# Optimization experiments

Hardware: AMD Instinct MI355X
Metric: run time of the kernel (lower is better)

## Reference

```python
import jax, jax.numpy as jnp
import numpy as np

SCALE = 20.0
MAX_Q = 256        # SwiGLUDiv max_quotient
MAX_SHIFT = 32     # SwiGLUShift max_shift
MEM_SIZE = 16777216

# c4 VM opcode numbering (39 opcodes; only these are gated in step)
LEA, IMM, JMP, JSR, BZ, BNZ, ENT, ADJ, LEV, LI, LC, SI, SC, PSH = range(14)
OR, XOR, AND, EQ, NE, LT, GT, LE, GE, SHL, SHR, ADD, SUB, MUL, DIV, MOD = range(14, 30)


def silu(x):
    return x * jax.nn.sigmoid(x)


def silu_threshold(x, s=SCALE):
    d = s * x
    return (silu(d + 0.5 * s) - silu(d - 0.5 * s)) / s


def swiglu_mul(a, b):
    return a * silu(b) - a * silu(-b)


def eq_gate(a, b, s=SCALE):
    diff = a - b
    return silu_threshold(diff + 0.5, s) * silu_threshold(-diff + 0.5, s)


def ge_gate(a, b, s=SCALE):
    return silu_threshold(a - b + 0.5, s)


def gt_gate(a, b, s=SCALE):
    return silu_threshold(a - b - 0.5, s)


def swiglu_div(a, b, s=SCALE):
    # division via quotient enumeration, vectorized over q (torch looped)
    q = jnp.arange(MAX_Q, dtype=jnp.float32)
    t1 = a - q * b + 0.5
    th1 = (silu(s * (t1 + 0.5)) - silu(s * (t1 - 0.5))) / s
    t2 = a - (q + 1.0) * b + 0.5
    th2 = (silu(s * (t2 + 0.5)) - silu(s * (t2 - 0.5))) / s
    return jnp.sum((th1 - th2) * q)


def _pulse(x, c):
    d = x - c
    return swiglu_mul(silu_threshold(d + 0.5), silu_threshold(-d + 0.5))


def left_shift(a, b):
    i = jnp.arange(MAX_SHIFT, dtype=jnp.float32)
    powers = 2.0 ** i
    return jnp.sum(swiglu_mul(a, powers) * _pulse(b, i))


def right_shift(a, b):
    i = jnp.arange(MAX_SHIFT, dtype=jnp.float32)
    powers = 2.0 ** i
    return jnp.sum(jnp.floor(a / powers) * _pulse(b, i))


def read_memory(memory, addr):
    # soft-attention read: torch looped over memory positions; vectorized here
    pos = jnp.arange(memory.shape[0], dtype=jnp.float32)
    w = eq_gate(addr, pos)
    w = w / (w.sum() + 1e-8)
    return jnp.sum(w * memory)


def write_memory(memory, addr, value):
    # soft-scatter write: lerp each slot by its address gate
    pos = jnp.arange(memory.shape[0], dtype=jnp.float32)
    g = eq_gate(addr, pos)
    return memory * (1.0 - g) + value * g


def _step(pc, sp, bp, ax, memory):
    pc, sp, bp, ax = (pc.astype(jnp.float32), sp.astype(jnp.float32),
                      bp.astype(jnp.float32), ax.astype(jnp.float32))
    memory = memory.astype(jnp.float32)

    instruction = read_memory(memory, pc)
    opcode = jnp.remainder(instruction, 256.0)
    imm = jnp.floor(instruction / 256.0)
    pc_next = pc + 8.0
    stack_top = read_memory(memory, sp)

    add_result = stack_top + ax
    sub_result = stack_top - ax
    mul_result = swiglu_mul(stack_top, ax)
    ax_safe = ax + eq_gate(ax, 0.0)
    div_result = swiglu_div(stack_top, ax_safe)
    mod_result = stack_top - swiglu_mul(div_result, ax_safe)
    shl_result = left_shift(stack_top, ax)
    shr_result = right_shift(stack_top, ax)
    or_result = stack_top + ax - swiglu_mul(stack_top, ax)
    xor_result = stack_top + ax - 2.0 * swiglu_mul(stack_top, ax)
    and_result = swiglu_mul(stack_top, ax)
    eq_result = eq_gate(stack_top, ax)
    ne_result = 1.0 - eq_gate(stack_top, ax)
    lt_result = gt_gate(ax, stack_top)
    gt_result = gt_gate(stack_top, ax)
    le_result = ge_gate(ax, stack_top)
    ge_result = ge_gate(stack_top, ax)
    li_result = read_memory(memory, ax)
    lc_result = read_memory(memory, ax)
    lea_result = bp + imm

    g = lambda op: eq_gate(opcode, float(op))
    g_lea, g_imm, g_li, g_lc = g(LEA), g(IMM), g(LI), g(LC)
    g_add, g_sub, g_mul, g_div, g_mod = g(ADD), g(SUB), g(MUL), g(DIV), g(MOD)
    g_shl, g_shr, g_or, g_xor, g_and = g(SHL), g(SHR), g(OR), g(XOR), g(AND)
    g_eq, g_ne, g_lt, g_gt, g_le, g_ge = g(EQ), g(NE), g(LT), g(GT), g(LE), g(GE)

    gate_sum = (g_lea + g_imm + g_li + g_lc + g_add + g_sub + g_mul + g_div
                + g_mod + g_shl + g_shr + g_or + g_xor + g_and + g_eq + g_ne
                + g_lt + g_gt + g_le + g_ge)
    new_ax = (ax * (1.0 - gate_sum)
              + lea_result * g_lea + imm * g_imm + li_result * g_li + lc_result * g_lc
              + add_result * g_add + sub_result * g_sub + mul_result * g_mul
              + div_result * g_div + mod_result * g_mod + shl_result * g_shl
              + shr_result * g_shr + or_result * g_or + xor_result * g_xor
              + and_result * g_and + eq_result * g_eq + ne_result * g_ne
              + lt_result * g_lt + gt_result * g_gt + le_result * g_le + ge_result * g_ge)

    g_psh, g_adj, g_ent, g_lev = g(PSH), g(ADJ), g(ENT), g(LEV)
    pops = (g_add + g_sub + g_mul + g_div + g_mod + g_shl + g_shr + g_or + g_xor
            + g_and + g_eq + g_ne + g_lt + g_gt + g_le + g_ge)
    new_sp = (sp * (1.0 - g_psh - g_adj - g_ent - g_lev - pops)
              + (sp - 8.0) * g_psh + (sp + imm) * g_adj + (sp - imm) * g_ent
              + bp * g_lev + (sp + 8.0) * pops)

    bp_from_stack = read_memory(memory, bp)
    new_bp = bp * (1.0 - g_ent - g_lev) + sp * g_ent + bp_from_stack * g_lev

    g_jmp, g_jsr, g_bz, g_bnz = g(JMP), g(JSR), g(BZ), g(BNZ)
    bz_take = swiglu_mul(g_bz, eq_gate(ax, 0.0))
    bnz_take = swiglu_mul(g_bnz, 1.0 - eq_gate(ax, 0.0))
    pc_from_stack = read_memory(memory, sp + 8.0)
    new_pc = (pc_next * (1.0 - g_jmp - g_jsr - bz_take - bnz_take - g_lev)
              + imm * g_jmp + imm * g_jsr + imm * bz_take + imm * bnz_take
              + pc_from_stack * g_lev)

    new_memory = memory
    new_memory = write_memory(new_memory, (sp - 8.0) * g_psh, ax * g_psh)
    new_memory = write_memory(new_memory, (sp - 8.0) * g_jsr, pc_next * g_jsr)
    new_memory = write_memory(new_memory, (sp - 8.0) * g_ent, bp * g_ent)
    g_si, g_sc = g(SI), g(SC)
    new_memory = write_memory(new_memory, stack_top * g_si, ax * g_si)
    new_memory = write_memory(new_memory, stack_top * g_sc, ax * g_sc)

    return (jnp.round(new_pc), jnp.round(new_sp), jnp.round(new_bp),
            jnp.round(new_ax), new_memory)


def setup_inputs() -> dict:
    key = jax.random.key(0)
    k_mem, = jax.random.split(key, 1)
    # memory holds integer-valued floats (instructions/data)
    memory = jnp.round(jax.random.normal(k_mem, (MEM_SIZE,), dtype=jnp.float32) * 100.0)
    pc = jnp.asarray(0.0, jnp.float32)
    sp = jnp.asarray(float(MEM_SIZE - 64), jnp.float32)
    bp = jnp.asarray(float(MEM_SIZE - 64), jnp.float32)
    ax = jnp.asarray(8.0, jnp.float32)
    return {"pc": pc, "sp": sp, "bp": bp, "ax": ax, "memory": memory}


def reference(pc, sp, bp, ax, memory):
    return _step(pc, sp, bp, ax, memory)
```

## Files before the change

### kernel.cpp

```cpp
#include <hip/hip_runtime.h>

#define MEM_SIZE 16777216
#define N4 (MEM_SIZE / 4)


__device__ __forceinline__ float silu_f(float x) {
    return x / (1.0f + __expf(-x));
}

__device__ __forceinline__ float silu_th(float x) {
    float d = 20.0f * x;
    return (silu_f(d + 10.0f) - silu_f(d - 10.0f)) * 0.05f;
}

__device__ __forceinline__ float eq_g(float a, float b) {
    float diff = a - b;
    return silu_th(diff + 0.5f) * silu_th(0.5f - diff);
}
__device__ __forceinline__ float ge_g(float a, float b) { return silu_th(a - b + 0.5f); }
__device__ __forceinline__ float gt_g(float a, float b) { return silu_th(a - b - 0.5f); }

__device__ __forceinline__ float swiglu_mul_f(float a, float b) {
    return a * silu_f(b) - a * silu_f(-b);
}

__device__ __forceinline__ float pulse_f(float x, float c) {
    float d = x - c;
    return swiglu_mul_f(silu_th(d + 0.5f), silu_th(0.5f - d));
}

__device__ float read_mem_soft(const float* mem, float addr) {
    float ca = rintf(addr);
    if (!(ca > -16.0f && ca < (float)MEM_SIZE + 16.0f)) return 0.0f;
    int c = (int)ca;
    float wsum = 0.0f, vsum = 0.0f;
    for (int d = -5; d <= 5; ++d) {
        int i = c + d;
        if (i < 0 || i >= MEM_SIZE) continue;
        float w = eq_g(addr, (float)i);
        wsum += w;
        vsum += w * mem[i];
    }
    return vsum / (wsum + 1e-8f);
}

__global__ __launch_bounds__(256) void k_copy(const float* __restrict__ mem,
                                              float* __restrict__ out) {
    const float4* __restrict__ src = (const float4*)mem;
    float4* __restrict__ dst = (float4*)(out + 4);
    int stride = (int)gridDim.x * 256;
    for (int i = (int)blockIdx.x * 256 + (int)threadIdx.x; i < N4; i += stride)
        dst[i] = src[i];
}

__global__ __launch_bounds__(256) void k_step(
    const float* __restrict__ pc_p, const float* __restrict__ sp_p,
    const float* __restrict__ bp_p, const float* __restrict__ ax_p,
    const float* __restrict__ mem, float* __restrict__ out)
{
    __shared__ float s_reads[5];
    __shared__ float sred[256];
    __shared__ float sres[3];
    __shared__ float s_ws[10];
    int t = threadIdx.x;

    float pc = pc_p[0], sp = sp_p[0], bp = bp_p[0], ax = ax_p[0];

    if (t < 5) {
        float addr = (t == 0) ? pc
                   : (t == 1) ? sp
                   : (t == 2) ? ax
                   : (t == 3) ? bp
                              : (sp + 8.0f);
        s_reads[t] = read_mem_soft(mem, addr);
    }
    __syncthreads();

    float instruction   = s_reads[0];
    float stack_top     = s_reads[1];
    float li_result     = s_reads[2];
    float bp_from_stack = s_reads[3];
    float pc_from_stack = s_reads[4];

    float ax_safe = ax + eq_g(ax, 0.0f);

    {
        float q  = (float)t;
        float t1 = stack_top - q * ax_safe + 0.5f;
        float t2 = stack_top - (q + 1.0f) * ax_safe + 0.5f;
        sred[t] = (silu_th(t1) - silu_th(t2)) * q;
    }
    __syncthreads();
    for (int off = 128; off >= 1; off >>= 1) {
        if (t < off) sred[t] += sred[t + off];
        __syncthreads();
    }
    if (t == 0) sres[0] = sred[0];
    __syncthreads();

    float shlterm = 0.0f, shrterm = 0.0f;
    if (t < 32) {
        float p  = ldexpf(1.0f, t);
        float pl = pulse_f(ax, (float)t);
        shlterm = swiglu_mul_f(stack_top, p) * pl;
        shrterm = floorf(stack_top / p) * pl;
    }
    sred[t] = shlterm;
    __syncthreads();
    for (int off = 128; off >= 1; off >>= 1) {
        if (t < off) sred[t] += sred[t + off];
        __syncthreads();
    }
    if (t == 0) sres[1] = sred[0];
    __syncthreads();
    sred[t] = shrterm;
    __syncthreads();
    for (int off = 128; off >= 1; off >>= 1) {
        if (t < off) sred[t] += sred[t + off];
        __syncthreads();
    }
    if (t == 0) sres[2] = sred[0];
    __syncthreads();

    if (t == 0) {
        float pc_next = pc + 8.0f;
        float imm     = floorf(instruction * (1.0f / 256.0f));
        float opcode  = instruction - imm * 256.0f;

        float add_result = stack_top + ax;
        float sub_result = stack_top - ax;
        float mul_result = swiglu_mul_f(stack_top, ax);
        float div_result = sres[0];
        float mod_result = stack_top - swiglu_mul_f(div_result, ax_safe);
        float shl_result = sres[1];
        float shr_result = sres[2];
        float or_result  = stack_top + ax - swiglu_mul_f(stack_top, ax);
        float xor_result = stack_top + ax - 2.0f * swiglu_mul_f(stack_top, ax);
        float and_result = swiglu_mul_f(stack_top, ax);
        float eq_result  = eq_g(stack_top, ax);
        float ne_result  = 1.0f - eq_g(stack_top, ax);
        float lt_result  = gt_g(ax, stack_top);
        float gt_result  = gt_g(stack_top, ax);
        float le_result  = ge_g(ax, stack_top);
        float ge_result  = ge_g(stack_top, ax);
        float lc_result  = li_result;
        float lea_result = bp + imm;

        float g_lea = eq_g(opcode, 0.0f),  g_imm = eq_g(opcode, 1.0f);
        float g_jmp = eq_g(opcode, 2.0f),  g_jsr = eq_g(opcode, 3.0f);
        float g_bz  = eq_g(opcode, 4.0f),  g_bnz = eq_g(opcode, 5.0f);
        float g_ent = eq_g(opcode, 6.0f),  g_adj = eq_g(opcode, 7.0f);
        float g_lev = eq_g(opcode, 8.0f),  g_li  = eq_g(opcode, 9.0f);
        float g_lc  = eq_g(opcode, 10.0f), g_si  = eq_g(opcode, 11.0f);
        float g_sc  = eq_g(opcode, 12.0f), g_psh = eq_g(opcode, 13.0f);
        float g_or  = eq_g(opcode, 14.0f), g_xor = eq_g(opcode, 15.0f);
        float g_and = eq_g(opcode, 16.0f), g_eq  = eq_g(opcode, 17.0f);
        float g_ne  = eq_g(opcode, 18.0f), g_lt  = eq_g(opcode, 19.0f);
        float g_gt  = eq_g(opcode, 20.0f), g_le  = eq_g(opcode, 21.0f);
        float g_ge  = eq_g(opcode, 22.0f), g_shl = eq_g(opcode, 23.0f);
        float g_shr = eq_g(opcode, 24.0f), g_add = eq_g(opcode, 25.0f);
        float g_sub = eq_g(opcode, 26.0f), g_mul = eq_g(opcode, 27.0f);
        float g_div = eq_g(opcode, 28.0f), g_mod = eq_g(opcode, 29.0f);

        float gate_sum = g_lea + g_imm + g_li + g_lc + g_add + g_sub + g_mul + g_div
                       + g_mod + g_shl + g_shr + g_or + g_xor + g_and + g_eq + g_ne
                       + g_lt + g_gt + g_le + g_ge;
        float new_ax = ax * (1.0f - gate_sum)
            + lea_result * g_lea + imm * g_imm + li_result * g_li + lc_result * g_lc
            + add_result * g_add + sub_result * g_sub + mul_result * g_mul
            + div_result * g_div + mod_result * g_mod + shl_result * g_shl
            + shr_result * g_shr + or_result * g_or + xor_result * g_xor
            + and_result * g_and + eq_result * g_eq + ne_result * g_ne
            + lt_result * g_lt + gt_result * g_gt + le_result * g_le + ge_result * g_ge;

        float pops = g_add + g_sub + g_mul + g_div + g_mod + g_shl + g_shr + g_or + g_xor
                   + g_and + g_eq + g_ne + g_lt + g_gt + g_le + g_ge;
        float new_sp = sp * (1.0f - g_psh - g_adj - g_ent - g_lev - pops)
            + (sp - 8.0f) * g_psh + (sp + imm) * g_adj + (sp - imm) * g_ent
            + bp * g_lev + (sp + 8.0f) * pops;

        float new_bp = bp * (1.0f - g_ent - g_lev) + sp * g_ent + bp_from_stack * g_lev;

        float eq_ax0   = eq_g(ax, 0.0f);
        float bz_take  = swiglu_mul_f(g_bz, eq_ax0);
        float bnz_take = swiglu_mul_f(g_bnz, 1.0f - eq_ax0);
        float new_pc = pc_next * (1.0f - g_jmp - g_jsr - bz_take - bnz_take - g_lev)
            + imm * g_jmp + imm * g_jsr + imm * bz_take + imm * bnz_take
            + pc_from_stack * g_lev;

        out[0] = rintf(new_pc);
        out[1] = rintf(new_sp);
        out[2] = rintf(new_bp);
        out[3] = rintf(new_ax);

        s_ws[0] = (sp - 8.0f) * g_psh;  s_ws[1] = ax * g_psh;
        s_ws[2] = (sp - 8.0f) * g_jsr;  s_ws[3] = pc_next * g_jsr;
        s_ws[4] = (sp - 8.0f) * g_ent;  s_ws[5] = bp * g_ent;
        s_ws[6] = stack_top * g_si;     s_ws[7] = ax * g_si;
        s_ws[8] = stack_top * g_sc;     s_ws[9] = ax * g_sc;
    }
    __syncthreads();

    const int R = 6, W = 2 * R + 1;
    if (t >= 5 * W) return;
    int j = t / W;
    int d = t % W - R;

    float cj = rintf(s_ws[2 * j]);
    if (!(cj > -64.0f && cj < (float)MEM_SIZE + 64.0f)) return;
    int slot = (int)cj + d;
    if (slot < 0 || slot >= MEM_SIZE) return;

    for (int j2 = 0; j2 < j; ++j2) {
        float c2 = rintf(s_ws[2 * j2]);
        if (c2 > -64.0f && c2 < (float)MEM_SIZE + 64.0f) {
            int cc = (int)c2;
            if (slot >= cc - R && slot <= cc + R) return;
        }
    }

    float fs = (float)slot;
    float m = out[4 + slot];
    #pragma unroll
    for (int jj = 0; jj < 5; ++jj) {
        float a = s_ws[2 * jj], v = s_ws[2 * jj + 1];
        float g = eq_g(a, fs);
        m = m * (1.0f - g) + v * g;
    }
    out[4 + slot] = m;
}

extern "C" void kernel_launch(void* const* d_in, const int* in_sizes, int n_in,
                              void* d_out, int out_size, void* d_ws, size_t ws_size,
                              hipStream_t stream) {
    const float* pc  = (const float*)d_in[0];
    const float* sp  = (const float*)d_in[1];
    const float* bp  = (const float*)d_in[2];
    const float* ax  = (const float*)d_in[3];
    const float* mem = (const float*)d_in[4];
    float* out = (float*)d_out;

    hipLaunchKernelGGL(k_copy, dim3(4096), dim3(256), 0, stream, mem, out);
    hipLaunchKernelGGL(k_step, dim3(1), dim3(256), 0, stream,
                       pc, sp, bp, ax, mem, out);
}
```

Baseline: 133.6 us.

## Fuse copy and VM step into one kernel with last-block completion counter

```diff
diff --git a/kernel.cpp b/kernel.cpp
--- a/kernel.cpp
+++ b/kernel.cpp
@@ -2,6 +2,9 @@
 
 #define MEM_SIZE 16777216
 #define N4 (MEM_SIZE / 4)
+#define COPY_BLOCKS 4096
+
+typedef float floatx4 __attribute__((ext_vector_type(4)));
 
 
 __device__ __forceinline__ float silu_f(float x) {
@@ -44,190 +47,210 @@
     return vsum / (wsum + 1e-8f);
 }
 
-__global__ __launch_bounds__(256) void k_copy(const float* __restrict__ mem,
-                                              float* __restrict__ out) {
-    const float4* __restrict__ src = (const float4*)mem;
-    float4* __restrict__ dst = (float4*)(out + 4);
-    int stride = (int)gridDim.x * 256;
-    for (int i = (int)blockIdx.x * 256 + (int)threadIdx.x; i < N4; i += stride)
-        dst[i] = src[i];
-}
-
-__global__ __launch_bounds__(256) void k_step(
+__global__ __launch_bounds__(256) void k_fused(
     const float* __restrict__ pc_p, const float* __restrict__ sp_p,
     const float* __restrict__ bp_p, const float* __restrict__ ax_p,
-    const float* __restrict__ mem, float* __restrict__ out)
+    const float* __restrict__ mem, float* __restrict__ out,
+    float* __restrict__ ws)
 {
-    __shared__ float s_reads[5];
-    __shared__ float sred[256];
-    __shared__ float sres[3];
+    unsigned int* counter = (unsigned int*)ws;
+    float* wsd = ws + 16;
+
     __shared__ float s_ws[10];
+    __shared__ unsigned int s_last;
     int t = threadIdx.x;
 
-    float pc = pc_p[0], sp = sp_p[0], bp = bp_p[0], ax = ax_p[0];
-
-    if (t < 5) {
-        float addr = (t == 0) ? pc
-                   : (t == 1) ? sp
-                   : (t == 2) ? ax
-                   : (t == 3) ? bp
-                              : (sp + 8.0f);
-        s_reads[t] = read_mem_soft(mem, addr);
-    }
+    if (blockIdx.x != 0) {
+        const floatx4* __restrict__ src = (const floatx4*)mem;
+        floatx4* __restrict__ dst = (floatx4*)(out + 4);
+        int stride = COPY_BLOCKS * 256;
+        for (int i = ((int)blockIdx.x - 1) * 256 + t; i < N4; i += stride) {
+            floatx4 v = __builtin_nontemporal_load(&src[i]);
+            __builtin_nontemporal_store(v, &dst[i]);
+        }
+    } else {
+        __shared__ float s_reads[5];
+        __shared__ float sred[256];
+        __shared__ float sres[3];
+
+        float pc = pc_p[0], sp = sp_p[0], bp = bp_p[0], ax = ax_p[0];
+
+        if (t < 5) {
+            float addr = (t == 0) ? pc
+                       : (t == 1) ? sp
+                       : (t == 2) ? ax
+                       : (t == 3) ? bp
+                                  : (sp + 8.0f);
+            s_reads[t] = read_mem_soft(mem, addr);
+        }
+        __syncthreads();
+
+        float instruction   = s_reads[0];
+        float stack_top     = s_reads[1];
+        float li_result     = s_reads[2];
+        float bp_from_stack = s_reads[3];
+        float pc_from_stack = s_reads[4];
+
+        float ax_safe = ax + eq_g(ax, 0.0f);
+
+        {
+            float q  = (float)t;
+            float t1 = stack_top - q * ax_safe + 0.5f;
+            float t2 = stack_top - (q + 1.0f) * ax_safe + 0.5f;
+            sred[t] = (silu_th(t1) - silu_th(t2)) * q;
+        }
+        __syncthreads();
+        for (int off = 128; off >= 1; off >>= 1) {
+            if (t < off) sred[t] += sred[t + off];
+            __syncthreads();
+        }
+        if (t == 0) sres[0] = sred[0];
+        __syncthreads();
+
+        float shlterm = 0.0f, shrterm = 0.0f;
+        if (t < 32) {
+            float p  = ldexpf(1.0f, t);
+            float pl = pulse_f(ax, (float)t);
+            shlterm = swiglu_mul_f(stack_top, p) * pl;
+            shrterm = floorf(stack_top / p) * pl;
+        }
+        sred[t] = shlterm;
+        __syncthreads();
+        for (int off = 128; off >= 1; off >>= 1) {
+            if (t < off) sred[t] += sred[t + off];
+            __syncthreads();
+        }
+        if (t == 0) sres[1] = sred[0];
+        __syncthreads();
+        sred[t] = shrterm;
+        __syncthreads();
+        for (int off = 128; off >= 1; off >>= 1) {
+            if (t < off) sred[t] += sred[t + off];
+            __syncthreads();
+        }
+        if (t == 0) sres[2] = sred[0];
+        __syncthreads();
+
+        if (t == 0) {
+            float pc_next = pc + 8.0f;
+            float imm     = floorf(instruction * (1.0f / 256.0f));
+            float opcode  = instruction - imm * 256.0f;
+
+            float add_result = stack_top + ax;
+            float sub_result = stack_top - ax;
+            float mul_result = swiglu_mul_f(stack_top, ax);
+            float div_result = sres[0];
+            float mod_result = stack_top - swiglu_mul_f(div_result, ax_safe);
+            float shl_result = sres[1];
+            float shr_result = sres[2];
+            float or_result  = stack_top + ax - swiglu_mul_f(stack_top, ax);
+            float xor_result = stack_top + ax - 2.0f * swiglu_mul_f(stack_top, ax);
+            float and_result = swiglu_mul_f(stack_top, ax);
+            float eq_result  = eq_g(stack_top, ax);
+            float ne_result  = 1.0f - eq_g(stack_top, ax);
+            float lt_result  = gt_g(ax, stack_top);
+            float gt_result  = gt_g(stack_top, ax);
+            float le_result  = ge_g(ax, stack_top);
+            float ge_result  = ge_g(stack_top, ax);
+            float lc_result  = li_result;
+            float lea_result = bp + imm;
+
+            float g_lea = eq_g(opcode, 0.0f),  g_imm = eq_g(opcode, 1.0f);
+            float g_jmp = eq_g(opcode, 2.0f),  g_jsr = eq_g(opcode, 3.0f);
+            float g_bz  = eq_g(opcode, 4.0f),  g_bnz = eq_g(opcode, 5.0f);
+            float g_ent = eq_g(opcode, 6.0f),  g_adj = eq_g(opcode, 7.0f);
+            float g_lev = eq_g(opcode, 8.0f),  g_li  = eq_g(opcode, 9.0f);
+            float g_lc  = eq_g(opcode, 10.0f), g_si  = eq_g(opcode, 11.0f);
+            float g_sc  = eq_g(opcode, 12.0f), g_psh = eq_g(opcode, 13.0f);
+            float g_or  = eq_g(opcode, 14.0f), g_xor = eq_g(opcode, 15.0f);
+            float g_and = eq_g(opcode, 16.0f), g_eq  = eq_g(opcode, 17.0f);
+            float g_ne  = eq_g(opcode, 18.0f), g_lt  = eq_g(opcode, 19.0f);
+            float g_gt  = eq_g(opcode, 20.0f), g_le  = eq_g(opcode, 21.0f);
+            float g_ge  = eq_g(opcode, 22.0f), g_shl = eq_g(opcode, 23.0f);
+            float g_shr = eq_g(opcode, 24.0f), g_add = eq_g(opcode, 25.0f);
+            float g_sub = eq_g(opcode, 26.0f), g_mul = eq_g(opcode, 27.0f);
+            float g_div = eq_g(opcode, 28.0f), g_mod = eq_g(opcode, 29.0f);
+
+            float gate_sum = g_lea + g_imm + g_li + g_lc + g_add + g_sub + g_mul + g_div
+                           + g_mod + g_shl + g_shr + g_or + g_xor + g_and + g_eq + g_ne
+                           + g_lt + g_gt + g_le + g_ge;
+            float new_ax = ax * (1.0f - gate_sum)
+                + lea_result * g_lea + imm * g_imm + li_result * g_li + lc_result * g_lc
+                + add_result * g_add + sub_result * g_sub + mul_result * g_mul
+                + div_result * g_div + mod_result * g_mod + shl_result * g_shl
+                + shr_result * g_shr + or_result * g_or + xor_result * g_xor
+                + and_result * g_and + eq_result * g_eq + ne_result * g_ne
+                + lt_result * g_lt + gt_result * g_gt + le_result * g_le + ge_result * g_ge;
+
+            float pops = g_add + g_sub + g_mul + g_div + g_mod + g_shl + g_shr + g_or + g_xor
+                       + g_and + g_eq + g_ne + g_lt + g_gt + g_le + g_ge;
+            float new_sp = sp * (1.0f - g_psh - g_adj - g_ent - g_lev - pops)
+                + (sp - 8.0f) * g_psh + (sp + imm) * g_adj + (sp - imm) * g_ent
+                + bp * g_lev + (sp + 8.0f) * pops;
+
+            float new_bp = bp * (1.0f - g_ent - g_lev) + sp * g_ent + bp_from_stack * g_lev;
+
+            float eq_ax0   = eq_g(ax, 0.0f);
+            float bz_take  = swiglu_mul_f(g_bz, eq_ax0);
+            float bnz_take = swiglu_mul_f(g_bnz, 1.0f - eq_ax0);
+            float new_pc = pc_next * (1.0f - g_jmp - g_jsr - bz_take - bnz_take - g_lev)
+                + imm * g_jmp + imm * g_jsr + imm * bz_take + imm * bnz_take
+                + pc_from_stack * g_lev;
+
+            out[0] = rintf(new_pc);
+            out[1] = rintf(new_sp);
+            out[2] = rintf(new_bp);
+            out[3] = rintf(new_ax);
+
+            wsd[0] = (sp - 8.0f) * g_psh;  wsd[1] = ax * g_psh;
+            wsd[2] = (sp - 8.0f) * g_jsr;  wsd[3] = pc_next * g_jsr;
+            wsd[4] = (sp - 8.0f) * g_ent;  wsd[5] = bp * g_ent;
+            wsd[6] = stack_top * g_si;     wsd[7] = ax * g_si;
+            wsd[8] = stack_top * g_sc;     wsd[9] = ax * g_sc;
+        }
+    }
+
     __syncthreads();
-
-    float instruction   = s_reads[0];
-    float stack_top     = s_reads[1];
-    float li_result     = s_reads[2];
-    float bp_from_stack = s_reads[3];
-    float pc_from_stack = s_reads[4];
-
-    float ax_safe = ax + eq_g(ax, 0.0f);
-
-    {
-        float q  = (float)t;
-        float t1 = stack_top - q * ax_safe + 0.5f;
-        float t2 = stack_top - (q + 1.0f) * ax_safe + 0.5f;
-        sred[t] = (silu_th(t1) - silu_th(t2)) * q;
+    if (t == 0) {
+        unsigned int old = __hip_atomic_fetch_add(counter, 1u,
+                                                  __ATOMIC_ACQ_REL,
+                                                  __HIP_MEMORY_SCOPE_AGENT);
+        s_last = (old == (unsigned int)gridDim.x - 1u) ? 1u : 0u;
     }
     __syncthreads();
-    for (int off = 128; off >= 1; off >>= 1) {
-        if (t < off) sred[t] += sred[t + off];
-        __syncthreads();
-    }
-    if (t == 0) sres[0] = sred[0];
-    __syncthreads();
-
-    float shlterm = 0.0f, shrterm = 0.0f;
-    if (t < 32) {
-        float p  = ldexpf(1.0f, t);
-        float pl = pulse_f(ax, (float)t);
-        shlterm = swiglu_mul_f(stack_top, p) * pl;
-        shrterm = floorf(stack_top / p) * pl;
-    }
-    sred[t] = shlterm;
-    __syncthreads();
-    for (int off = 128; off >= 1; off >>= 1) {
-        if (t < off) sred[t] += sred[t + off];
-        __syncthreads();
-    }
-    if (t == 0) sres[1] = sred[0];
-    __syncthreads();
-    sred[t] = shrterm;
-    __syncthreads();
-    for (int off = 128; off >= 1; off >>= 1) {
-        if (t < off) sred[t] += sred[t + off];
-        __syncthreads();
-    }
-    if (t == 0) sres[2] = sred[0];
-    __syncthreads();
-
-    if (t == 0) {
-        float pc_next = pc + 8.0f;
-        float imm     = floorf(instruction * (1.0f / 256.0f));
-        float opcode  = instruction - imm * 256.0f;
-
-        float add_result = stack_top + ax;
-        float sub_result = stack_top - ax;
-        float mul_result = swiglu_mul_f(stack_top, ax);
-        float div_result = sres[0];
-        float mod_result = stack_top - swiglu_mul_f(div_result, ax_safe);
-        float shl_result = sres[1];
-        float shr_result = sres[2];
-        float or_result  = stack_top + ax - swiglu_mul_f(stack_top, ax);
-        float xor_result = stack_top + ax - 2.0f * swiglu_mul_f(stack_top, ax);
-        float and_result = swiglu_mul_f(stack_top, ax);
-        float eq_result  = eq_g(stack_top, ax);
-        float ne_result  = 1.0f - eq_g(stack_top, ax);
-        float lt_result  = gt_g(ax, stack_top);
-        float gt_result  = gt_g(stack_top, ax);
-        float le_result  = ge_g(ax, stack_top);
-        float ge_result  = ge_g(stack_top, ax);
-        float lc_result  = li_result;
-        float lea_result = bp + imm;
-
-        float g_lea = eq_g(opcode, 0.0f),  g_imm = eq_g(opcode, 1.0f);
-        float g_jmp = eq_g(opcode, 2.0f),  g_jsr = eq_g(opcode, 3.0f);
-        float g_bz  = eq_g(opcode, 4.0f),  g_bnz = eq_g(opcode, 5.0f);
-        float g_ent = eq_g(opcode, 6.0f),  g_adj = eq_g(opcode, 7.0f);
-        float g_lev = eq_g(opcode, 8.0f),  g_li  = eq_g(opcode, 9.0f);
-        float g_lc  = eq_g(opcode, 10.0f), g_si  = eq_g(opcode, 11.0f);
-        float g_sc  = eq_g(opcode, 12.0f), g_psh = eq_g(opcode, 13.0f);
-        float g_or  = eq_g(opcode, 14.0f), g_xor = eq_g(opcode, 15.0f);
-        float g_and = eq_g(opcode, 16.0f), g_eq  = eq_g(opcode, 17.0f);
-        float g_ne  = eq_g(opcode, 18.0f), g_lt  = eq_g(opcode, 19.0f);
-        float g_gt  = eq_g(opcode, 20.0f), g_le  = eq_g(opcode, 21.0f);
-        float g_ge  = eq_g(opcode, 22.0f), g_shl = eq_g(opcode, 23.0f);
-        float g_shr = eq_g(opcode, 24.0f), g_add = eq_g(opcode, 25.0f);
-        float g_sub = eq_g(opcode, 26.0f), g_mul = eq_g(opcode, 27.0f);
-        float g_div = eq_g(opcode, 28.0f), g_mod = eq_g(opcode, 29.0f);
-
-        float gate_sum = g_lea + g_imm + g_li + g_lc + g_add + g_sub + g_mul + g_div
-                       + g_mod + g_shl + g_shr + g_or + g_xor + g_and + g_eq + g_ne
-                       + g_lt + g_gt + g_le + g_ge;
-        float new_ax = ax * (1.0f - gate_sum)
-            + lea_result * g_lea + imm * g_imm + li_result * g_li + lc_result * g_lc
-            + add_result * g_add + sub_result * g_sub + mul_result * g_mul
-            + div_result * g_div + mod_result * g_mod + shl_result * g_shl
-            + shr_result * g_shr + or_result * g_or + xor_result * g_xor
-            + and_result * g_and + eq_result * g_eq + ne_result * g_ne
-            + lt_result * g_lt + gt_result * g_gt + le_result * g_le + ge_result * g_ge;
-
-        float pops = g_add + g_sub + g_mul + g_div + g_mod + g_shl + g_shr + g_or + g_xor
-                   + g_and + g_eq + g_ne + g_lt + g_gt + g_le + g_ge;
-        float new_sp = sp * (1.0f - g_psh - g_adj - g_ent - g_lev - pops)
-            + (sp - 8.0f) * g_psh + (sp + imm) * g_adj + (sp - imm) * g_ent
-            + bp * g_lev + (sp + 8.0f) * pops;
-
-        float new_bp = bp * (1.0f - g_ent - g_lev) + sp * g_ent + bp_from_stack * g_lev;
-
-        float eq_ax0   = eq_g(ax, 0.0f);
-        float bz_take  = swiglu_mul_f(g_bz, eq_ax0);
-        float bnz_take = swiglu_mul_f(g_bnz, 1.0f - eq_ax0);
-        float new_pc = pc_next * (1.0f - g_jmp - g_jsr - bz_take - bnz_take - g_lev)
-            + imm * g_jmp + imm * g_jsr + imm * bz_take + imm * bnz_take
-            + pc_from_stack * g_lev;
-
-        out[0] = rintf(new_pc);
-        out[1] = rintf(new_sp);
-        out[2] = rintf(new_bp);
-        out[3] = rintf(new_ax);
-
-        s_ws[0] = (sp - 8.0f) * g_psh;  s_ws[1] = ax * g_psh;
-        s_ws[2] = (sp - 8.0f) * g_jsr;  s_ws[3] = pc_next * g_jsr;
-        s_ws[4] = (sp - 8.0f) * g_ent;  s_ws[5] = bp * g_ent;
-        s_ws[6] = stack_top * g_si;     s_ws[7] = ax * g_si;
-        s_ws[8] = stack_top * g_sc;     s_ws[9] = ax * g_sc;
-    }
-    __syncthreads();
-
-    const int R = 6, W = 2 * R + 1;
-    if (t >= 5 * W) return;
-    int j = t / W;
-    int d = t % W - R;
-
-    float cj = rintf(s_ws[2 * j]);
-    if (!(cj > -64.0f && cj < (float)MEM_SIZE + 64.0f)) return;
-    int slot = (int)cj + d;
-    if (slot < 0 || slot >= MEM_SIZE) return;
-
-    for (int j2 = 0; j2 < j; ++j2) {
-        float c2 = rintf(s_ws[2 * j2]);
-        if (c2 > -64.0f && c2 < (float)MEM_SIZE + 64.0f) {
-            int cc = (int)c2;
-            if (slot >= cc - R && slot <= cc + R) return;
-        }
-    }
-
-    float fs = (float)slot;
-    float m = out[4 + slot];
-    #pragma unroll
-    for (int jj = 0; jj < 5; ++jj) {
-        float a = s_ws[2 * jj], v = s_ws[2 * jj + 1];
-        float g = eq_g(a, fs);
-        m = m * (1.0f - g) + v * g;
-    }
-    out[4 + slot] = m;
+
+    if (s_last) {
+        if (t < 10) s_ws[t] = wsd[t];
+        __syncthreads();
+
+        const int R = 6, W = 2 * R + 1;
+        if (t >= 5 * W) return;
+        int j = t / W;
+        int d = t % W - R;
+
+        float cj = rintf(s_ws[2 * j]);
+        if (!(cj > -64.0f && cj < (float)MEM_SIZE + 64.0f)) return;
+        int slot = (int)cj + d;
+        if (slot < 0 || slot >= MEM_SIZE) return;
+
+        for (int j2 = 0; j2 < j; ++j2) {
+            float c2 = rintf(s_ws[2 * j2]);
+            if (c2 > -64.0f && c2 < (float)MEM_SIZE + 64.0f) {
+                int cc = (int)c2;
+                if (slot >= cc - R && slot <= cc + R) return;
+            }
+        }
+
+        float fs = (float)slot;
+        float m = mem[slot];
+        #pragma unroll
+        for (int jj = 0; jj < 5; ++jj) {
+            float a = s_ws[2 * jj], v = s_ws[2 * jj + 1];
+            float g = eq_g(a, fs);
+            m = m * (1.0f - g) + v * g;
+        }
+        out[4 + slot] = m;
+    }
 }
 
 extern "C" void kernel_launch(void* const* d_in, const int* in_sizes, int n_in,
@@ -239,8 +262,9 @@
     const float* ax  = (const float*)d_in[3];
     const float* mem = (const float*)d_in[4];
     float* out = (float*)d_out;
-
-    hipLaunchKernelGGL(k_copy, dim3(4096), dim3(256), 0, stream, mem, out);
-    hipLaunchKernelGGL(k_step, dim3(1), dim3(256), 0, stream,
-                       pc, sp, bp, ax, mem, out);
-}
+    float* ws  = (float*)d_ws;
+
+    (void)hipMemsetAsync(ws, 0, sizeof(unsigned int), stream);
+    hipLaunchKernelGGL(k_fused, dim3(COPY_BLOCKS + 1), dim3(256), 0, stream,
+                       pc, sp, bp, ax, mem, out, ws);
+}
```

Measured after the change: 310.5 us. +132.4%, slower.

## Fuse memory copy and VM step into one launch with disjoint write windows

Applied to the files above, without the earlier changes.

```diff
diff --git a/kernel.cpp b/kernel.cpp
--- a/kernel.cpp
+++ b/kernel.cpp
@@ -2,6 +2,7 @@
 
 #define MEM_SIZE 16777216
 #define N4 (MEM_SIZE / 4)
+#define COPY_BLOCKS 4096
 
 
 __device__ __forceinline__ float silu_f(float x) {
@@ -44,25 +45,56 @@
     return vsum / (wsum + 1e-8f);
 }
 
-__global__ __launch_bounds__(256) void k_copy(const float* __restrict__ mem,
-                                              float* __restrict__ out) {
-    const float4* __restrict__ src = (const float4*)mem;
-    float4* __restrict__ dst = (float4*)(out + 4);
-    int stride = (int)gridDim.x * 256;
-    for (int i = (int)blockIdx.x * 256 + (int)threadIdx.x; i < N4; i += stride)
-        dst[i] = src[i];
-}
-
-__global__ __launch_bounds__(256) void k_step(
+__device__ __forceinline__ void win4(int c, bool valid, int& lo4, int& hi4) {
+    if (!valid) { lo4 = 1; hi4 = 0; return; }
+    int a = c - 7, b = c + 7;
+    lo4 = (a >= 0) ? (a >> 2) : -(((-a) + 3) >> 2);
+    hi4 = (b >= 0) ? (b >> 2) : -(((-b) + 3) >> 2);
+    if (lo4 < 0) lo4 = 0;
+    if (hi4 > N4 - 1) hi4 = N4 - 1;
+    if (lo4 > hi4) { lo4 = 1; hi4 = 0; }
+}
+
+__device__ void calc_windows(const float* sp_p, const float* mem,
+                             int lo[3], int hi[3]) {
+    float sp = sp_p[0];
+    win4(0, true, lo[0], hi[0]);
+    float c1f = rintf(sp - 8.0f);
+    bool v1 = (c1f > -32.0f && c1f < (float)MEM_SIZE + 32.0f);
+    win4(v1 ? (int)c1f : 0, v1, lo[1], hi[1]);
+    float spr = rintf(sp);
+    bool spv = (spr >= 0.0f && spr < (float)MEM_SIZE);
+    float stf = spv ? rintf(mem[(int)spr]) : 0.0f;
+    bool v2 = spv && (stf > -32.0f && stf < (float)MEM_SIZE + 32.0f);
+    win4(v2 ? (int)stf : 0, v2, lo[2], hi[2]);
+}
+
+__global__ __launch_bounds__(256) void k_fused(
     const float* __restrict__ pc_p, const float* __restrict__ sp_p,
     const float* __restrict__ bp_p, const float* __restrict__ ax_p,
     const float* __restrict__ mem, float* __restrict__ out)
 {
+    int t = threadIdx.x;
+
+    if (blockIdx.x != 0) {
+        int lo[3], hi[3];
+        calc_windows(sp_p, mem, lo, hi);
+        const float4* __restrict__ src = (const float4*)mem;
+        float4* __restrict__ dst = (float4*)(out + 4);
+        int stride = COPY_BLOCKS * 256;
+        for (int i = ((int)blockIdx.x - 1) * 256 + t; i < N4; i += stride) {
+            bool skip = (i >= lo[0] && i <= hi[0]) ||
+                        (i >= lo[1] && i <= hi[1]) ||
+                        (i >= lo[2] && i <= hi[2]);
+            if (!skip) dst[i] = src[i];
+        }
+        return;
+    }
+
     __shared__ float s_reads[5];
     __shared__ float sred[256];
     __shared__ float sres[3];
     __shared__ float s_ws[10];
-    int t = threadIdx.x;
 
     float pc = pc_p[0], sp = sp_p[0], bp = bp_p[0], ax = ax_p[0];
 
@@ -201,26 +233,20 @@
     }
     __syncthreads();
 
-    const int R = 6, W = 2 * R + 1;
-    if (t >= 5 * W) return;
-    int j = t / W;
-    int d = t % W - R;
-
-    float cj = rintf(s_ws[2 * j]);
-    if (!(cj > -64.0f && cj < (float)MEM_SIZE + 64.0f)) return;
-    int slot = (int)cj + d;
-    if (slot < 0 || slot >= MEM_SIZE) return;
-
-    for (int j2 = 0; j2 < j; ++j2) {
-        float c2 = rintf(s_ws[2 * j2]);
-        if (c2 > -64.0f && c2 < (float)MEM_SIZE + 64.0f) {
-            int cc = (int)c2;
-            if (slot >= cc - R && slot <= cc + R) return;
-        }
-    }
+    int lo[3], hi[3];
+    calc_windows(sp_p, mem, lo, hi);
+
+    int w = t >> 5, k = t & 31;
+    if (w >= 3) return;
+    if (lo[w] > hi[w]) return;
+    int slot = lo[w] * 4 + k;
+    if (slot > hi[w] * 4 + 3) return;
+    for (int w2 = 0; w2 < w; ++w2)
+        if (lo[w2] <= hi[w2] && slot >= lo[w2] * 4 && slot <= hi[w2] * 4 + 3)
+            return;
 
     float fs = (float)slot;
-    float m = out[4 + slot];
+    float m = mem[slot];
     #pragma unroll
     for (int jj = 0; jj < 5; ++jj) {
         float a = s_ws[2 * jj], v = s_ws[2 * jj + 1];
@@ -240,7 +266,6 @@
     const float* mem = (const float*)d_in[4];
     float* out = (float*)d_out;
 
-    hipLaunchKernelGGL(k_copy, dim3(4096), dim3(256), 0, stream, mem, out);
-    hipLaunchKernelGGL(k_step, dim3(1), dim3(256), 0, stream,
+    hipLaunchKernelGGL(k_fused, dim3(COPY_BLOCKS + 1), dim3(256), 0, stream,
                        pc, sp, bp, ax, mem, out);
 }
```

Result: faster. 122.1 us (-8.6%).
